# Optimization experiments

Measured on AMD Instinct MI355X. Metric: run time of the kernel, lower is better.

The kernel has to match this reference:

```python
import jax, jax.numpy as jnp
import numpy as np
from jax import lax

K = 3          # kernel_size
G = 2          # num_groups
DN = ('NHWC', 'HWIO', 'NHWC')


def _conv_same(x, w, b, groups=1):
    y = lax.conv_general_dilated(x, w, (1, 1), 'SAME',
                                 dimension_numbers=DN,
                                 feature_group_count=groups)
    return y + b


def _kernel_grid():
    off = (K - 1) / 2.0
    lin = jnp.linspace(-off, off, K, dtype=jnp.float32)
    dx, dy = jnp.meshgrid(lin, lin)              # 'xy' indexing, like tf default
    return jnp.stack([dx, dy], axis=-1).reshape(K * K, 2)  # [K2, 2] (dx, dy)


def _bilinear_sample(inp, loc):
    # inp: [B,H,W,C], loc: [B,H,W,K2,2] with (x,y) already clipped to valid range
    B, H, W, C = inp.shape
    x, y = loc[..., 0], loc[..., 1]
    x0 = jnp.floor(x); y0 = jnp.floor(y)
    x1 = jnp.clip(x0 + 1.0, 0.0, W - 1.0); x0 = jnp.clip(x0, 0.0, W - 1.0)
    y1 = jnp.clip(y0 + 1.0, 0.0, H - 1.0); y0 = jnp.clip(y0, 0.0, H - 1.0)
    # corner weights (computed from clipped coords, matching the TF code)
    wa = (x1 - x) * (y1 - y)
    wb = (x1 - x) * (y - y0)
    wc = (x - x0) * (y1 - y)
    wd = (x - x0) * (y - y0)
    x0i = x0.astype(jnp.int32); x1i = x1.astype(jnp.int32)
    y0i = y0.astype(jnp.int32); y1i = y1.astype(jnp.int32)
    flat = inp.reshape(B, H * W, C)

    def gather(yi, xi):
        idx = (yi * W + xi).reshape(B, -1, 1)               # [B, H*W*K2, 1]
        v = jnp.take_along_axis(flat, idx, axis=1)          # [B, H*W*K2, C]
        return v.reshape(B, H, W, K * K, C)

    out = (wa[..., None] * gather(y0i, x0i) + wb[..., None] * gather(y1i, x0i)
           + wc[..., None] * gather(y0i, x1i) + wd[..., None] * gather(y1i, x1i))
    return out  # [B,H,W,K2,C]


def _forward(x, off_w, off_b, dw_w, dw_b, pw_w, pw_b):
    B, H, W, C = x.shape
    Cg = C // G
    kg = _kernel_grid()                                     # [K2,2]
    gx, gy = jnp.meshgrid(jnp.arange(W, dtype=jnp.float32),
                          jnp.arange(H, dtype=jnp.float32))
    grid = jnp.stack([gx, gy], axis=-1)                     # [H,W,2] (x,y)
    outs = []
    for g in range(G):
        xi = x[..., g * Cg:(g + 1) * Cg]                    # [B,H,W,Cg]
        offsets = _conv_same(xi, off_w[g], off_b[g])        # [B,H,W,2*K2]
        offsets = offsets.reshape(B, H, W, K * K, 2)
        loc = grid[None, :, :, None, :] + kg[None, None, None] + offsets
        loc = jnp.stack([jnp.clip(loc[..., 0], 0.0, W - 1.0),
                         jnp.clip(loc[..., 1], 0.0, H - 1.0)], axis=-1)
        sampled = _bilinear_sample(xi, loc)                 # [B,H,W,K2,Cg]
        Kin = K * K * Cg
        s = sampled.reshape(B, H, W, Kin)
        s = _conv_same(s, dw_w[g], dw_b[g], groups=Kin)     # depthwise 3x3
        s = _conv_same(s, pw_w[g], pw_b[g])                 # 1x1 pointwise
        outs.append(s)
    return jnp.concatenate(outs, axis=-1)


def setup_inputs() -> dict:
    key = jax.random.key(0)
    ks = jax.random.split(key, 6)
    B, H, W, C = 4, 128, 128, 128
    Cg = C // G
    F = 128
    Fg = F // G
    Kin = K * K * Cg
    x = jax.random.normal(ks[0], (B, H, W, C), jnp.float32)
    # offset conv (zero-init in source; small random weights so offsets ~1px)
    off_w = jax.random.normal(ks[1], (G, K, K, Cg, 2 * K * K), jnp.float32) * 0.05
    off_b = jnp.zeros((G, 2 * K * K), jnp.float32)
    dw_w = jax.random.normal(ks[2], (G, K, K, 1, Kin), jnp.float32) * 0.1
    dw_b = jnp.zeros((G, Kin), jnp.float32)
    pw_w = jax.random.normal(ks[3], (G, 1, 1, Kin, Fg), jnp.float32) / np.sqrt(Kin)
    pw_b = jnp.zeros((G, Fg), jnp.float32)
    return {"x": x, "off_w": off_w, "off_b": off_b,
            "dw_w": dw_w, "dw_b": dw_b, "pw_w": pw_w, "pw_b": pw_b}


def reference(x, off_w, off_b, dw_w, dw_b, pw_w, pw_b):
    return _forward(x, off_w, off_b, dw_w, dw_b, pw_w, pw_b)
```

## Files before the change

### kernel.cpp

```cpp
#include <hip/hip_runtime.h>
#include <hip/hip_bf16.h>

#define HW 128
#define GNUM 2
#define BATCH 4
#define OBT_STRIDE (GNUM * 18 * 2 * 512)
#define PWT_FLOATS 36864
#define OBT_FLOATS 36864
#define DWP_WORDS 5184

typedef short s16x8 __attribute__((ext_vector_type(8)));
typedef _Float16 f16x8 __attribute__((ext_vector_type(8)));
typedef _Float16 f16x2 __attribute__((ext_vector_type(2)));
typedef __fp16 h16x2 __attribute__((ext_vector_type(2)));
typedef float f32x4 __attribute__((ext_vector_type(4)));
typedef float f32x2 __attribute__((ext_vector_type(2)));

__device__ inline unsigned short f2bf(float f) {
    union { float f; unsigned u; } v;
    v.f = f;
    unsigned r = (v.u + 0x7fffu + ((v.u >> 16) & 1u)) >> 16;
    return (unsigned short)r;
}
__device__ inline unsigned pk2bf(float lo, float hi) {
    __hip_bfloat162 r = __float22bfloat162_rn(float2{lo, hi});
    return *(unsigned*)&r;
}
__device__ inline float blo(unsigned u) {
    union { unsigned u; float f; } v; v.u = u << 16; return v.f;
}
__device__ inline float bhi(unsigned u) {
    union { unsigned u; float f; } v; v.u = u & 0xffff0000u; return v.f;
}
__device__ inline unsigned short f2h(float f) {
    _Float16 h = (_Float16)f;
    return *(unsigned short*)&h;
}
__device__ inline unsigned pk2h(float lo, float hi) {
    union { h16x2 h; unsigned u; } v;
    v.h = __builtin_amdgcn_cvt_pkrtz(lo, hi);
    return v.u;
}
__device__ inline f16x2 u2h(unsigned u) {
    union { unsigned u; f16x2 h; } v; v.u = u; return v.h;
}
__device__ inline unsigned h2u(f16x2 h) {
    union { unsigned u; f16x2 h; } v; v.h = h; return v.u;
}
__device__ inline int swz(int row, int off) {
    return (off & 7) | ((((off >> 3) ^ (row + (row >> 3))) & 7) << 3);
}

__global__ __launch_bounds__(256) void prep_kernel(
    const float* __restrict__ pw_w, const float* __restrict__ dw_b,
    const float* __restrict__ off_w, const float* __restrict__ dw_w,
    unsigned short* __restrict__ pwt, unsigned short* __restrict__ obt,
    unsigned* __restrict__ dwp, float* __restrict__ bias2) {
    const int g = blockIdx.y;
    const int t = threadIdx.x;
    if (blockIdx.x < 9) {
        const int j = blockIdx.x;
        const int wv = t >> 6, lane = t & 63;
        const int f = wv * 16 + (lane & 15);
        const int kbase = (lane >> 4) << 3;
#pragma unroll
        for (int ks = 0; ks < 2; ++ks)
#pragma unroll
            for (int i = 0; i < 8; ++i) {
                int kin = j * 64 + ks * 32 + kbase + i;
                pwt[((((g * 9 + j) * 4 + wv) * 2 + ks) << 9) + lane * 8 + i] =
                    f2h(pw_w[(g * 576 + kin) * 64 + f]);
            }
        for (int e = t; e < 288; e += 256) {
            int tap2 = e >> 5, cp = e & 31;
            const float* dwr = &dw_w[(g * 9 + tap2) * 576 + (j << 6) + cp * 2];
            dwp[(((g * 9 + tap2) * 9 + j) << 5) + cp] = pk2h(dwr[0], dwr[1]);
        }
    } else if (blockIdx.x < 27) {
        const int s = blockIdx.x - 9;
        const int tap = s >> 1;
        for (int e = t; e < 1024; e += 256) {
            int nt = e >> 9, le = e & 511;
            int lane = le >> 3, i = le & 7;
            int k = ((lane >> 4) << 3) + i;
            int c = ((s & 1) << 5) + k;
            int n = (nt << 4) + (lane & 15);
            float v = (n < 18) ? off_w[((g * 9 + tap) * 64 + c) * 18 + n] : 0.f;
            unsigned short hi = f2bf(v);
            unsigned short lo = f2bf(v - blo(hi));
            int idx = (((g * 18 + s) * 2 + nt) << 9) + le;
            obt[idx] = hi;
            obt[OBT_STRIDE + idx] = lo;
        }
    } else {
        if (t < 64) {
            float s = 0.f;
            for (int kin = 0; kin < 576; ++kin)
                s += pw_w[(g * 576 + kin) * 64 + t] * dw_b[g * 576 + kin];
            bias2[g * 64 + t] = s;
        }
    }
}

__global__ __launch_bounds__(256, 4) void deform_fused(
    const float* __restrict__ x, const unsigned short* __restrict__ obt,
    const float* __restrict__ off_b, const unsigned* __restrict__ dwp,
    const unsigned short* __restrict__ pwt, const float* __restrict__ bias2,
    const float* __restrict__ pw_b, float* __restrict__ out) {
    __shared__ char smem[38992];
    unsigned short* xh = (unsigned short*)smem;
    float* offs = (float*)smem;
    unsigned short* samp = (unsigned short*)smem;
    unsigned short* dwa = (unsigned short*)(smem + 12800);
    float4* wlwAll = (float4*)(smem + 20992);
    unsigned* wliAll = (unsigned*)(smem + 35392);

    const int b = blockIdx.x >> 1, g = blockIdx.x & 1;
    const int tileIdx = blockIdx.y;
    const int h0 = (tileIdx >> 4) << 3, w0 = (tileIdx & 15) << 3;
    const int t = threadIdx.x;
    const int lane = t & 63;
    const int wv = __builtin_amdgcn_readfirstlane(t >> 6);
    const int kq = (lane >> 4) << 3;
    const int col = lane & 15;
    const int rq = (lane >> 4) << 2;

    f32x4 oacc[2][2];
#pragma unroll
    for (int sl = 0; sl < 2; ++sl)
#pragma unroll
        for (int nt = 0; nt < 2; ++nt) oacc[sl][nt] = (f32x4){0.f, 0.f, 0.f, 0.f};
    int mbase[2];
#pragma unroll
    for (int sl = 0; sl < 2; ++sl) {
        int mt = wv + (sl << 2);
        int m = mt * 16 + col;
        if (mt < 7 && m < 100) {
            int opy = m / 10, opx = m - opy * 10;
            mbase[sl] = opy * 12 + opx;
        } else
            mbase[sl] = 0;
    }
    for (int q = 0; q < 2; ++q) {
        if (q) __syncthreads();
        for (int idx = t; idx < 144 * 8; idx += 256) {
            int sp = idx >> 3, cq = idx & 7;
            int sy = sp / 12, sx = sp - sy * 12;
            int gy = h0 - 2 + sy, gx = w0 - 2 + sx;
            uint2 hp = {0, 0}, lp = {0, 0};
            if ((unsigned)gy < HW && (unsigned)gx < HW) {
                const float4 v = *(const float4*)&x[(((b * HW + gy) * HW + gx)
                                                    << 7) +
                                                   (g << 6) + (q << 5) + (cq << 2)];
                hp.x = pk2bf(v.x, v.y);
                hp.y = pk2bf(v.z, v.w);
                lp.x = pk2bf(v.x - blo(hp.x), v.y - bhi(hp.x));
                lp.y = pk2bf(v.z - blo(hp.y), v.w - bhi(hp.y));
            }
            *(uint2*)&xh[sp * 64 + swz(sp, cq << 2)] = hp;
            *(uint2*)&xh[sp * 64 + swz(sp, 32 + (cq << 2))] = lp;
        }
        __syncthreads();
        for (int tap = 0; tap < 9; ++tap) {
            const int s = (tap << 1) + q;
            const int ky = tap / 3, kx = tap - ky * 3;
            const int shift = ky * 12 + kx;
            const int bidx = ((g * 18 + s) << 1) << 9;
            s16x8 bh0 = *(const s16x8*)&obt[bidx + lane * 8];
            s16x8 bh1 = *(const s16x8*)&obt[bidx + 512 + lane * 8];
            s16x8 bl0 = *(const s16x8*)&obt[OBT_STRIDE + bidx + lane * 8];
            s16x8 bl1 = *(const s16x8*)&obt[OBT_STRIDE + bidx + 512 + lane * 8];
#pragma unroll
            for (int sl = 0; sl < 2; ++sl) {
                if (wv + (sl << 2) < 7) {
                    const int m2 = mbase[sl] + shift;
                    s16x8 ah = *(const s16x8*)&xh[m2 * 64 + swz(m2, kq)];
                    s16x8 al = *(const s16x8*)&xh[m2 * 64 + swz(m2, kq + 32)];
                    oacc[sl][0] = __builtin_amdgcn_mfma_f32_16x16x32_bf16(
                        ah, bh0, oacc[sl][0], 0, 0, 0);
                    oacc[sl][1] = __builtin_amdgcn_mfma_f32_16x16x32_bf16(
                        ah, bh1, oacc[sl][1], 0, 0, 0);
                    oacc[sl][0] = __builtin_amdgcn_mfma_f32_16x16x32_bf16(
                        al, bh0, oacc[sl][0], 0, 0, 0);
                    oacc[sl][1] = __builtin_amdgcn_mfma_f32_16x16x32_bf16(
                        al, bh1, oacc[sl][1], 0, 0, 0);
                    oacc[sl][0] = __builtin_amdgcn_mfma_f32_16x16x32_bf16(
                        ah, bl0, oacc[sl][0], 0, 0, 0);
                    oacc[sl][1] = __builtin_amdgcn_mfma_f32_16x16x32_bf16(
                        ah, bl1, oacc[sl][1], 0, 0, 0);
                }
            }
        }
    }
    __syncthreads();
#pragma unroll
    for (int sl = 0; sl < 2; ++sl) {
        int mt = wv + (sl << 2);
        if (mt < 7) {
#pragma unroll
            for (int nt = 0; nt < 2; ++nt) {
                int o = (nt << 4) + col;
                if (o < 18) {
                    float ob = off_b[g * 18 + o];
#pragma unroll
                    for (int i = 0; i < 4; ++i) {
                        int m = mt * 16 + rq + i;
                        if (m < 100) offs[m * 18 + o] = oacc[sl][nt][i] + ob;
                    }
                }
            }
        }
    }
    __syncthreads();
    for (int e = t; e < 900; e += 256) {
        const int jj = e / 100, sp = e - jj * 100;
        const int jy = jj / 3, jx = jj - jy * 3;
        const int spy = sp / 10, spx = sp - spy * 10;
        const int gy = h0 - 1 + spy, gx = w0 - 1 + spx;
        float4 w4 = {0.f, 0.f, 0.f, 0.f};
        unsigned wp = (unsigned)(b << 21);
        if ((unsigned)gy < HW && (unsigned)gx < HW) {
            const float ox = offs[sp * 18 + 2 * jj];
            const float oy = offs[sp * 18 + 2 * jj + 1];
            float xf = fminf(fmaxf((float)(gx + jx - 1) + ox, 0.f), 127.f);
            float yf = fminf(fmaxf((float)(gy + jy - 1) + oy, 0.f), 127.f);
            float x0 = floorf(xf), y0 = floorf(yf);
            float x1 = fminf(x0 + 1.f, 127.f);
            float y1 = fminf(y0 + 1.f, 127.f);
            w4.x = (x1 - xf) * (y1 - yf);
            w4.y = (x1 - xf) * (yf - y0);
            w4.z = (xf - x0) * (y1 - yf);
            w4.w = (xf - x0) * (yf - y0);
            const int x0i = (int)x0, y0i = (int)y0;
            wp = (unsigned)(((b * HW + y0i) * HW + x0i) << 7) |
                 (unsigned)((int)x1 - x0i) |
                 ((unsigned)((int)y1 - y0i) << 1);
        }
        wlwAll[jj * 100 + sp] = w4;
        wliAll[jj * 100 + sp] = wp;
    }
    __syncthreads();

    const int fb = wv << 4;
    const int p = lane;
    const int ayp = p >> 3, axp = p & 7;
    const int grp = t >> 4, sl16 = t & 15;
    const int prow = ayp * 10 + axp;

    int aoff[9][2];
#pragma unroll
    for (int t2 = 0; t2 < 9; ++t2) {
        const int ky = t2 / 3, kx = t2 - ky * 3;
        const int row = prow + ky * 10 + kx;
#pragma unroll
        for (int cq = 0; cq < 2; ++cq)
            aoff[t2][cq] = row * 64 + swz(row, fb + (cq << 3));
    }
    int doff[2];
#pragma unroll
    for (int cq = 0; cq < 2; ++cq) doff[cq] = p * 64 + swz(p, fb + (cq << 3));
    int boff[2][4];
#pragma unroll
    for (int ks = 0; ks < 2; ++ks)
#pragma unroll
        for (int mt = 0; mt < 4; ++mt) {
            const int row = mt * 16 + col;
            boff[ks][mt] = row * 64 + swz(row, ks * 32 + kq);
        }
    int soff[7];
#pragma unroll
    for (int it = 0; it < 7; ++it) {
        const int sp_ = (it << 4) + grp;
        soff[it] = sp_ * 64 + swz(sp_, sl16 << 2);
    }

    const float bs = bias2[g * 64 + fb + col] + pw_b[g * 64 + fb + col];
    f32x4 acc[4];
#pragma unroll
    for (int mt = 0; mt < 4; ++mt) acc[mt] = (f32x4){bs, bs, bs, bs};

    for (int j = 0; j < 9; ++j) {
        f16x8 bfr[2];
#pragma unroll
        for (int ks = 0; ks < 2; ++ks)
            bfr[ks] = *(const f16x8*)&pwt[((((g * 9 + j) * 4 + wv) * 2 + ks)
                                           << 9) + lane * 8];
        for (int it = 0; it < 7; ++it) {
            const int sp = (it << 4) + grp;
            if (sp < 100) {
                const float4 w4 = wlwAll[j * 100 + sp];
                const unsigned wp = wliAll[j * 100 + sp];
                const float* xa = x + (wp & 0xFFFFFF80u) + (g << 6) +
                                  (sl16 << 2);
                const int xo = (int)((wp & 1u) << 7);
                const int yo = (int)((wp & 2u) << 13);
                const float4 va = *(const float4*)xa;
                const float4 vb = *(const float4*)(xa + yo);
                const float4 vc = *(const float4*)(xa + xo);
                const float4 vd = *(const float4*)(xa + xo + yo);
                f32x2 a01 = {va.x, va.y}, b01 = {vb.x, vb.y};
                f32x2 c01 = {vc.x, vc.y}, d01 = {vd.x, vd.y};
                f32x2 a23 = {va.z, va.w}, b23 = {vb.z, vb.w};
                f32x2 c23 = {vc.z, vc.w}, d23 = {vd.z, vd.w};
                f32x2 r01 = w4.x * a01 + w4.y * b01 + w4.z * c01 + w4.w * d01;
                f32x2 r23 = w4.x * a23 + w4.y * b23 + w4.z * c23 + w4.w * d23;
                uint2 pk;
                pk.x = pk2h(r01.x, r01.y);
                pk.y = pk2h(r23.x, r23.y);
                *(uint2*)&samp[soff[it]] = pk;
            }
        }
        __syncthreads();
#pragma unroll
        for (int cq = 0; cq < 2; ++cq) {
            const int c8 = fb + (cq << 3);
            f16x2 d0 = {0, 0}, d1 = {0, 0}, d2 = {0, 0}, d3 = {0, 0};
#pragma unroll
            for (int t2 = 0; t2 < 9; ++t2) {
                const uint4 hv = *(const uint4*)&samp[aoff[t2][cq]];
                const uint4 wq =
                    *(const uint4*)&dwp[(((g * 9 + t2) * 9 + j) << 5) +
                                        (c8 >> 1)];
                d0 = u2h(hv.x) * u2h(wq.x) + d0;
                d1 = u2h(hv.y) * u2h(wq.y) + d1;
                d2 = u2h(hv.z) * u2h(wq.z) + d2;
                d3 = u2h(hv.w) * u2h(wq.w) + d3;
            }
            uint4 pk;
            pk.x = h2u(d0);
            pk.y = h2u(d1);
            pk.z = h2u(d2);
            pk.w = h2u(d3);
            *(uint4*)&dwa[doff[cq]] = pk;
        }
        __syncthreads();
#pragma unroll
        for (int ks = 0; ks < 2; ++ks)
#pragma unroll
            for (int mt = 0; mt < 4; ++mt) {
                f16x8 af = *(const f16x8*)&dwa[boff[ks][mt]];
                acc[mt] = __builtin_amdgcn_mfma_f32_16x16x32_f16(
                    af, bfr[ks], acc[mt], 0, 0, 0);
            }
    }
#pragma unroll
    for (int mt = 0; mt < 4; ++mt)
#pragma unroll
        for (int i = 0; i < 4; ++i) {
            int m = mt * 16 + rq + i;
            out[((b * HW + h0 + (m >> 3)) * HW + (w0 + (m & 7))) * 128 +
                (g << 6) + fb + col] = acc[mt][i];
        }
}

extern "C" void kernel_launch(void* const* d_in, const int* in_sizes, int n_in,
                              void* d_out, int out_size, void* d_ws,
                              size_t ws_size, hipStream_t stream) {
    const float* x = (const float*)d_in[0];
    const float* off_w = (const float*)d_in[1];
    const float* off_b = (const float*)d_in[2];
    const float* dw_w = (const float*)d_in[3];
    const float* dw_b = (const float*)d_in[4];
    const float* pw_w = (const float*)d_in[5];
    const float* pw_b = (const float*)d_in[6];

    float* wsf = (float*)d_ws;
    unsigned short* pwt = (unsigned short*)wsf;
    unsigned short* obt = (unsigned short*)(wsf + PWT_FLOATS);
    unsigned* dwp = (unsigned*)(wsf + PWT_FLOATS + OBT_FLOATS);
    float* bias2 = wsf + PWT_FLOATS + OBT_FLOATS + DWP_WORDS;

    prep_kernel<<<dim3(28, GNUM), dim3(256), 0, stream>>>(pw_w, dw_b, off_w,
                                                          dw_w, pwt, obt, dwp,
                                                          bias2);
    deform_fused<<<dim3(BATCH * GNUM, 256), dim3(256), 0, stream>>>(
        x, obt, off_b, dwp, pwt, bias2, pw_b, (float*)d_out);
}
```

Before: 209.1 us.

## Software-pipeline bilinear gather loads into registers one tap ahead

Global loads for the four bilinear corners of the next tap are issued into a register array (28 float4 per thread) before the barrier and the depthwise/MFMA stages of the current tap run, so gather latency overlaps with compute. Occupancy is lowered from 4 to 3 blocks per CU to make room for the extra registers, and some precomputed LDS offsets are now recomputed inline to save registers. Out-of-range lanes clamp their index to avoid branching in the prefetch. The trade-off is fewer resident waves to hide latency in exchange for explicit prefetching.

```diff
diff --git a/kernel.cpp b/kernel.cpp
--- a/kernel.cpp
+++ b/kernel.cpp
@@ -102,7 +102,22 @@
     }
 }
 
-__global__ __launch_bounds__(256, 4) void deform_fused(
+#define S_ISSUE(JJ)                                                          \
+    _Pragma("unroll")                                                        \
+    for (int it = 0; it < 7; ++it) {                                         \
+        int sp_ = (it << 4) + grp;                                           \
+        int spc = sp_ < 100 ? sp_ : 99;                                      \
+        unsigned wp = wliAll[(JJ) * 100 + spc];                              \
+        const float* xa = x + (wp & 0xFFFFFF80u) + (g << 6) + (sl16 << 2);   \
+        const int xo = (int)((wp & 1u) << 7);                                \
+        const int yo = (int)((wp & 2u) << 13);                               \
+        rv[it][0] = *(const float4*)xa;                                      \
+        rv[it][1] = *(const float4*)(xa + yo);                               \
+        rv[it][2] = *(const float4*)(xa + xo);                               \
+        rv[it][3] = *(const float4*)(xa + xo + yo);                          \
+    }
+
+__global__ __launch_bounds__(256, 3) void deform_fused(
     const float* __restrict__ x, const unsigned short* __restrict__ obt,
     const float* __restrict__ off_b, const unsigned* __restrict__ dwp,
     const unsigned short* __restrict__ pwt, const float* __restrict__ bias2,
@@ -256,9 +271,6 @@
         for (int cq = 0; cq < 2; ++cq)
             aoff[t2][cq] = row * 64 + swz(row, fb + (cq << 3));
     }
-    int doff[2];
-#pragma unroll
-    for (int cq = 0; cq < 2; ++cq) doff[cq] = p * 64 + swz(p, fb + (cq << 3));
     int boff[2][4];
 #pragma unroll
     for (int ks = 0; ks < 2; ++ks)
@@ -267,49 +279,43 @@
             const int row = mt * 16 + col;
             boff[ks][mt] = row * 64 + swz(row, ks * 32 + kq);
         }
-    int soff[7];
-#pragma unroll
-    for (int it = 0; it < 7; ++it) {
-        const int sp_ = (it << 4) + grp;
-        soff[it] = sp_ * 64 + swz(sp_, sl16 << 2);
-    }
 
     const float bs = bias2[g * 64 + fb + col] + pw_b[g * 64 + fb + col];
     f32x4 acc[4];
 #pragma unroll
     for (int mt = 0; mt < 4; ++mt) acc[mt] = (f32x4){bs, bs, bs, bs};
 
+    float4 rv[7][4];
+    S_ISSUE(0);
+
     for (int j = 0; j < 9; ++j) {
-        f16x8 bfr[2];
-#pragma unroll
-        for (int ks = 0; ks < 2; ++ks)
-            bfr[ks] = *(const f16x8*)&pwt[((((g * 9 + j) * 4 + wv) * 2 + ks)
-                                           << 9) + lane * 8];
+#pragma unroll
         for (int it = 0; it < 7; ++it) {
             const int sp = (it << 4) + grp;
-            if (sp < 100) {
+            if (it < 6 || grp < 4) {
                 const float4 w4 = wlwAll[j * 100 + sp];
-                const unsigned wp = wliAll[j * 100 + sp];
-                const float* xa = x + (wp & 0xFFFFFF80u) + (g << 6) +
-                                  (sl16 << 2);
-                const int xo = (int)((wp & 1u) << 7);
-                const int yo = (int)((wp & 2u) << 13);
-                const float4 va = *(const float4*)xa;
-                const float4 vb = *(const float4*)(xa + yo);
-                const float4 vc = *(const float4*)(xa + xo);
-                const float4 vd = *(const float4*)(xa + xo + yo);
-                f32x2 a01 = {va.x, va.y}, b01 = {vb.x, vb.y};
-                f32x2 c01 = {vc.x, vc.y}, d01 = {vd.x, vd.y};
-                f32x2 a23 = {va.z, va.w}, b23 = {vb.z, vb.w};
-                f32x2 c23 = {vc.z, vc.w}, d23 = {vd.z, vd.w};
+                f32x2 a01 = {rv[it][0].x, rv[it][0].y};
+                f32x2 b01 = {rv[it][1].x, rv[it][1].y};
+                f32x2 c01 = {rv[it][2].x, rv[it][2].y};
+                f32x2 d01 = {rv[it][3].x, rv[it][3].y};
+                f32x2 a23 = {rv[it][0].z, rv[it][0].w};
+                f32x2 b23 = {rv[it][1].z, rv[it][1].w};
+                f32x2 c23 = {rv[it][2].z, rv[it][2].w};
+                f32x2 d23 = {rv[it][3].z, rv[it][3].w};
                 f32x2 r01 = w4.x * a01 + w4.y * b01 + w4.z * c01 + w4.w * d01;
                 f32x2 r23 = w4.x * a23 + w4.y * b23 + w4.z * c23 + w4.w * d23;
                 uint2 pk;
                 pk.x = pk2h(r01.x, r01.y);
                 pk.y = pk2h(r23.x, r23.y);
-                *(uint2*)&samp[soff[it]] = pk;
-            }
-        }
+                *(uint2*)&samp[sp * 64 + swz(sp, sl16 << 2)] = pk;
+            }
+        }
+        if (j < 8) { S_ISSUE(j + 1); }
+        f16x8 bfr[2];
+#pragma unroll
+        for (int ks = 0; ks < 2; ++ks)
+            bfr[ks] = *(const f16x8*)&pwt[((((g * 9 + j) * 4 + wv) * 2 + ks)
+                                           << 9) + lane * 8];
         __syncthreads();
 #pragma unroll
         for (int cq = 0; cq < 2; ++cq) {
@@ -331,7 +337,7 @@
             pk.y = h2u(d1);
             pk.z = h2u(d2);
             pk.w = h2u(d3);
-            *(uint4*)&dwa[doff[cq]] = pk;
+            *(uint4*)&dwa[p * 64 + swz(p, c8)] = pk;
         }
         __syncthreads();
 #pragma unroll
```

After: 346.9 us. 65.9% more time.
